# Performance work log

Measured on AMD Instinct MI355X. Metric: run time of the kernel, lower is better.

Reference implementation:

```python
import jax, jax.numpy as jnp
import numpy as np

GAIN = 1.0
EPS = 1e-08


def setup_inputs() -> dict:
    key = jax.random.key(0)
    k1, k2, k3 = jax.random.split(key, 3)
    B, H, W, Cin, Cout, K = 8, 64, 64, 512, 512, 3
    x = jax.random.normal(k1, (B, H, W, Cin), dtype=jnp.float32)
    style = jax.random.normal(k2, (B, Cin), dtype=jnp.float32)
    kernel = jax.random.normal(k3, (K, K, Cin, Cout), dtype=jnp.float32)
    return {"x": x, "style": style, "kernel": kernel}


def reference(x, style, kernel):
    # x: [B,H,W,Cin], style: [B,Cin], kernel: [K,K,Cin,Cout]
    B, H, W, Cin = x.shape
    K = kernel.shape[0]
    Cout = kernel.shape[-1]
    scale = GAIN / np.sqrt(K * K * Cin)

    # modulate: per-sample weights [B,K,K,Cin,Cout]
    ww = (scale * kernel)[None] * style[:, None, None, :, None]
    # demodulate
    sigma = jax.lax.rsqrt(jnp.sum(jnp.square(ww), axis=(1, 2, 3)) + EPS)  # [B,Cout]
    ww = ww * sigma[:, None, None, None, :]

    # grouped conv via batch->channel reshape (groups = B)
    x_nchw = jnp.transpose(x, (0, 3, 1, 2)).reshape(1, B * Cin, H, W)
    # weights to HWIO with per-sample groups stacked on output channels
    w = jnp.transpose(ww, (1, 2, 3, 0, 4)).reshape(K, K, Cin, B * Cout)
    out = jax.lax.conv_general_dilated(
        x_nchw, w,
        window_strides=(1, 1),
        padding='SAME',
        dimension_numbers=('NCHW', 'HWIO', 'NCHW'),
        feature_group_count=B,
    )  # [1, B*Cout, H, W]
    out = out.reshape(B, Cout, H, W)
    return jnp.transpose(out, (0, 2, 3, 1))  # [B,H,W,Cout]
```

## Files before the change

### kernel.cpp

```cpp
#include <hip/hip_runtime.h>

typedef __bf16 bf16x8 __attribute__((ext_vector_type(8)));
typedef float f32x4 __attribute__((ext_vector_type(4)));

#define SCALE_F 0.014731391274719738f
#define SCALE2_F 2.170138888888889e-4f

__device__ __forceinline__ ushort f2bf(float f) {
    uint x = __float_as_uint(f);
    uint r = (x + 0x7fffu + ((x >> 16) & 1u)) >> 16;
    return (ushort)r;
}

__device__ __forceinline__ void async_cp16(const void* g, void* l) {
    __builtin_amdgcn_global_load_lds(
        (const __attribute__((address_space(1))) void*)g,
        (__attribute__((address_space(3))) void*)l, 16, 0, 0);
}


__global__ void k_q(const float* __restrict__ kern, float* __restrict__ Q) {
    int idx = blockIdx.x * 256 + threadIdx.x;
    float s = 0.f;
#pragma unroll
    for (int t = 0; t < 9; ++t) { float v = kern[t * 262144 + idx]; s += v * v; }
    Q[idx] = s * SCALE2_F;
}

__global__ void k_sigma(const float* __restrict__ style, const float* __restrict__ Q,
                        float* __restrict__ sig) {
    __shared__ float s2[512];
    int b = blockIdx.x, t = threadIdx.x;
    float s = style[b * 512 + t];
    s2[t] = s * s;
    __syncthreads();
    float acc = 0.f;
#pragma unroll 8
    for (int ci = 0; ci < 512; ++ci) acc += s2[ci] * Q[ci * 512 + t];
    sig[b * 512 + t] = rsqrtf(acc + 1e-8f);
}

__global__ void k_wt(const float* __restrict__ kern, const float* __restrict__ style,
                     const float* __restrict__ sig, ushort* __restrict__ wT) {
    __shared__ ushort tile[64 * 65];
    int b = blockIdx.z, tap = blockIdx.y;
    int ci0 = (blockIdx.x >> 3) << 6, co0 = (blockIdx.x & 7) << 6;
    int t = threadIdx.x;
    int col = t & 63, rq = t >> 6;
#pragma unroll
    for (int r = 0; r < 16; ++r) {
        int ci_l = r * 4 + rq;
        float v = kern[(size_t)(tap * 512 + ci0 + ci_l) * 512 + co0 + col];
        float val = SCALE_F * v * style[b * 512 + ci0 + ci_l] * sig[b * 512 + co0 + col];
        tile[ci_l * 65 + col] = f2bf(val);
    }
    __syncthreads();
#pragma unroll
    for (int r = 0; r < 4; ++r) {
        int q = r * 256 + t;
        int co_l = q >> 4, ciq = (q & 15) << 2;
        uint lo = (uint)tile[ciq * 65 + co_l] | ((uint)tile[(ciq + 1) * 65 + co_l] << 16);
        uint hi = (uint)tile[(ciq + 2) * 65 + co_l] | ((uint)tile[(ciq + 3) * 65 + co_l] << 16);
        *(uint2*)(&wT[((size_t)(b * 9 + tap) * 512 + co0 + co_l) * 512 + ci0 + ciq]) =
            make_uint2(lo, hi);
    }
}

__global__ void k_xpad(const float* __restrict__ x, ushort* __restrict__ xp) {
    int idx = blockIdx.x * 256 + threadIdx.x;
    int pos = idx >> 6, e = idx & 63;
    int b = pos / 4356, rem = pos - b * 4356;
    int hp = rem / 66, wp = rem - hp * 66;
    int ci0 = e << 3;
    uint4 o = make_uint4(0u, 0u, 0u, 0u);
    if (hp >= 1 && hp <= 64 && wp >= 1 && wp <= 64) {
        const float4* s =
            (const float4*)(x + (((size_t)(b * 4096 + (hp - 1) * 64 + (wp - 1))) << 9) + ci0);
        float4 v0 = s[0], v1 = s[1];
        o.x = (uint)f2bf(v0.x) | ((uint)f2bf(v0.y) << 16);
        o.y = (uint)f2bf(v0.z) | ((uint)f2bf(v0.w) << 16);
        o.z = (uint)f2bf(v1.x) | ((uint)f2bf(v1.y) << 16);
        o.w = (uint)f2bf(v1.z) | ((uint)f2bf(v1.w) << 16);
    }
    *(uint4*)(xp + (((size_t)pos) << 9) + ci0) = o;
}

__global__ __launch_bounds__(512, 2) void conv_mfma(const ushort* __restrict__ xpad,
                                                    const ushort* __restrict__ wT,
                                                    float* __restrict__ out) {
    extern __shared__ char lds[];

    const int wg = blockIdx.x;
    const int swz = (wg & 7) * 32 + (wg >> 3);
    const int mt = swz & 15;
    const int nt = (swz >> 4) & 1;
    const int b = swz >> 5;

    const int tid = threadIdx.x;
    const int l = tid & 63, wv = tid >> 6;
    const int wm = (wv >> 2) * 128;
    const int wn = (wv & 3) * 64;
    const int ha = wv >> 2;
    const int hb = (wv & 3) >> 1;

    const int rl = l >> 3;
    const int g = (l & 7) ^ rl;
    const ushort* baseA[2][2];
    const ushort* baseB[2][2];
#pragma unroll
    for (int h = 0; h < 2; ++h)
#pragma unroll
        for (int i = 0; i < 2; ++i) {
            int rloc = wv * 16 + i * 8 + rl;
            int R = h * 128 + rloc;
            baseA[h][i] = xpad + ((size_t)((b * 66 + mt * 4 + (R >> 6)) * 66 + (R & 63))) * 512 + g * 8;
            baseB[h][i] = wT + ((size_t)(b * 9 * 512 + nt * 256 + R)) * 512 + g * 8;
        }
    const int so0 = (wv * 16) * 128;
    const int so1 = (wv * 16 + 8) * 128;

    auto offA = [](int t) -> int {
        int tap = t >> 3;
        int ky = (tap * 11) >> 5;
        int kx = tap - ky * 3;
        return (ky * 66 + kx) * 512 + ((t & 7) << 6);
    };
    auto offB = [](int t) -> int { return (t >> 3) * 262144 + ((t & 7) << 6); };

    auto stA = [&](int t, int h) {
        int ts = t > 71 ? 71 : t;
        int o = offA(ts);
        char* d = lds + (t & 1) * 32768 + h * 16384;
        async_cp16(baseA[h][0] + o, d + so0);
        async_cp16(baseA[h][1] + o, d + so1);
    };
    auto stB = [&](int t, int h) {
        int ts = t > 71 ? 71 : t;
        int o = offB(ts);
        char* d = lds + 65536 + (t & 1) * 32768 + h * 16384;
        async_cp16(baseB[h][0] + o, d + so0);
        async_cp16(baseB[h][1] + o, d + so1);
    };

    const int frow = l & 15;
    const int fchunk_base = l >> 4;
    const int fxor = l & 7;

    f32x4 acc[8][4];
#pragma unroll
    for (int mi = 0; mi < 8; ++mi)
#pragma unroll
        for (int ni = 0; ni < 4; ++ni) acc[mi][ni] = (f32x4){0.f, 0.f, 0.f, 0.f};

    bf16x8 bq[4][2];
    bf16x8 aqE[2][2], aqO[2][2];

    auto rdB = [&](const char* bB) {
#pragma unroll
        for (int kk = 0; kk < 2; ++kk)
#pragma unroll
            for (int ni = 0; ni < 4; ++ni) {
                int r = (wn & 64) + ni * 16 + frow;
                bq[ni][kk] = *(const bf16x8*)(bB + r * 128 +
                                              (((kk * 4 + fchunk_base) ^ fxor) * 16));
            }
    };
    auto rdA = [&](bf16x8 (&aq)[2][2], const char* aB, int q) {
#pragma unroll
        for (int m2 = 0; m2 < 2; ++m2)
#pragma unroll
            for (int kk = 0; kk < 2; ++kk) {
                int r = (2 * q + m2) * 16 + frow;
                aq[m2][kk] = *(const bf16x8*)(aB + r * 128 +
                                              (((kk * 4 + fchunk_base) ^ fxor) * 16));
            }
    };

#define FENCE_L4                                                        \
    {                                                                   \
        __builtin_amdgcn_sched_barrier(0);                              \
        asm volatile("s_waitcnt lgkmcnt(4)" ::: "memory");              \
        __builtin_amdgcn_s_barrier();                                   \
        __builtin_amdgcn_sched_barrier(0);                              \
    }
#define FENCE_L12                                                       \
    {                                                                   \
        __builtin_amdgcn_sched_barrier(0);                              \
        asm volatile("s_waitcnt lgkmcnt(12)" ::: "memory");             \
        __builtin_amdgcn_s_barrier();                                   \
        __builtin_amdgcn_sched_barrier(0);                              \
    }
#define FENCE_V4L4                                                      \
    {                                                                   \
        __builtin_amdgcn_sched_barrier(0);                              \
        asm volatile("s_waitcnt vmcnt(4) lgkmcnt(4)" ::: "memory");     \
        __builtin_amdgcn_s_barrier();                                   \
        __builtin_amdgcn_sched_barrier(0);                              \
    }
#define FENCE_V2L4                                                      \
    {                                                                   \
        __builtin_amdgcn_sched_barrier(0);                              \
        asm volatile("s_waitcnt vmcnt(2) lgkmcnt(4)" ::: "memory");     \
        __builtin_amdgcn_s_barrier();                                   \
        __builtin_amdgcn_sched_barrier(0);                              \
    }

#define MFMA16(Q, AQ)                                                                  \
    do {                                                                               \
        __builtin_amdgcn_s_setprio(1);                                                 \
        _Pragma("unroll") for (int kk = 0; kk < 2; ++kk)                               \
            _Pragma("unroll") for (int ni = 0; ni < 4; ++ni)                           \
                _Pragma("unroll") for (int m2 = 0; m2 < 2; ++m2)                       \
                    acc[2 * (Q) + m2][ni] = __builtin_amdgcn_mfma_f32_16x16x32_bf16(   \
                        (AQ)[m2][kk], bq[ni][kk], acc[2 * (Q) + m2][ni], 0, 0, 0);     \
        __builtin_amdgcn_s_setprio(0);                                                 \
    } while (0)

    const char* Ab0 = lds + ha * 16384;
    const char* Ab1 = lds + 32768 + ha * 16384;
    const char* Bb0 = lds + 65536 + hb * 16384;
    const char* Bb1 = lds + 98304 + hb * 16384;

    stA(0, 0); stA(0, 1);
    stB(0, 0); stB(0, 1);
    asm volatile("s_waitcnt vmcnt(0)" ::: "memory");
    __builtin_amdgcn_sched_barrier(0);
    __builtin_amdgcn_s_barrier();
    __builtin_amdgcn_sched_barrier(0);
    stB(1, 0); stB(1, 1);
    rdA(aqE, Ab0, 0);
    rdB(Bb0);

#pragma unroll 1
    for (int i = 0; i < 36; ++i) {
        const int T = 2 * i;
        rdA(aqO, Ab0, 1); stA(T + 1, 0);
        FENCE_L12; MFMA16(0, aqE);
        rdA(aqE, Ab0, 2); stA(T + 1, 1);
        FENCE_V4L4; MFMA16(1, aqO);
        rdA(aqO, Ab0, 3); stB(T + 2, 0);
        FENCE_V2L4; MFMA16(2, aqE);
        rdA(aqE, Ab1, 0); stB(T + 2, 1);
        FENCE_L4; MFMA16(3, aqO);
        rdB(Bb1);
        rdA(aqO, Ab1, 1); stA(T + 2, 0);
        FENCE_L12; MFMA16(0, aqE);
        rdA(aqE, Ab1, 2); stA(T + 2, 1);
        FENCE_L4; MFMA16(1, aqO);
        rdA(aqO, Ab1, 3); stB(T + 3, 0);
        FENCE_V2L4; MFMA16(2, aqE);
        rdA(aqE, Ab0, 0); stB(T + 3, 1);
        FENCE_L4; MFMA16(3, aqO);
        rdB(Bb0);
    }

    asm volatile("s_waitcnt vmcnt(0) lgkmcnt(0)" ::: "memory");

#pragma unroll
    for (int mi = 0; mi < 8; ++mi) {
#pragma unroll
        for (int ni = 0; ni < 4; ++ni) {
#pragma unroll
            for (int r = 0; r < 4; ++r) {
                int m = mt * 256 + wm + mi * 16 + (l >> 4) * 4 + r;
                int co = nt * 256 + wn + ni * 16 + (l & 15);
                out[(((size_t)(b * 4096 + m)) << 9) + co] = acc[mi][ni][r];
            }
        }
    }
#undef MFMA16
#undef FENCE_L4
#undef FENCE_L12
#undef FENCE_V4L4
#undef FENCE_V2L4
}


extern "C" void kernel_launch(void* const* d_in, const int* in_sizes, int n_in,
                              void* d_out, int out_size, void* d_ws, size_t ws_size,
                              hipStream_t stream) {
    const float* x = (const float*)d_in[0];
    const float* style = (const float*)d_in[1];
    const float* kern = (const float*)d_in[2];
    float* out = (float*)d_out;

    char* ws = (char*)d_ws;
    ushort* xpad = (ushort*)ws;
    ushort* wT = (ushort*)(ws + 35684352);
    float* Q = (float*)(ws + 35684352 + 37748736);
    float* sig = (float*)(ws + 35684352 + 37748736 + 1048576);

    (void)hipFuncSetAttribute((const void*)conv_mfma,
                              hipFuncAttributeMaxDynamicSharedMemorySize, 131072);

    k_q<<<1024, 256, 0, stream>>>(kern, Q);
    k_sigma<<<8, 512, 0, stream>>>(style, Q, sig);
    k_wt<<<dim3(64, 9, 8), 256, 0, stream>>>(kern, style, sig, wT);
    k_xpad<<<8712, 256, 0, stream>>>(x, xpad);
    conv_mfma<<<256, 512, 131072, stream>>>(xpad, wT, out);
}
```

Before: 180.1 us.

## Switch conv to 32x32x16 MFMA and load kernel tile once per batch

The main conv kernel replaces 16x16x32 bf16 MFMA tiles with 32x32x16 tiles. The LDS fragment reads, accumulators and output indexing are reorganised to match, which means fewer MFMA issues and fewer LDS reads per unit of work. Separately, the weight-modulation kernel now loads each fp32 kernel tile once and loops over the 8 batch samples, instead of launching one block per sample that re-reads the kernel. This cuts global reads but serialises the per-batch work inside fewer blocks, and the new fragment layout risks LDS bank conflicts.

```diff
diff --git a/kernel.cpp b/kernel.cpp
--- a/kernel.cpp
+++ b/kernel.cpp
@@ -1,7 +1,7 @@
 #include <hip/hip_runtime.h>
 
 typedef __bf16 bf16x8 __attribute__((ext_vector_type(8)));
-typedef float f32x4 __attribute__((ext_vector_type(4)));
+typedef float f32x16 __attribute__((ext_vector_type(16)));
 
 #define SCALE_F 0.014731391274719738f
 #define SCALE2_F 2.170138888888889e-4f
@@ -42,27 +42,33 @@
 
 __global__ void k_wt(const float* __restrict__ kern, const float* __restrict__ style,
                      const float* __restrict__ sig, ushort* __restrict__ wT) {
-    __shared__ ushort tile[64 * 65];
-    int b = blockIdx.z, tap = blockIdx.y;
+    __shared__ float tile[64][65];
+    int tap = blockIdx.y;
     int ci0 = (blockIdx.x >> 3) << 6, co0 = (blockIdx.x & 7) << 6;
     int t = threadIdx.x;
     int col = t & 63, rq = t >> 6;
 #pragma unroll
     for (int r = 0; r < 16; ++r) {
         int ci_l = r * 4 + rq;
-        float v = kern[(size_t)(tap * 512 + ci0 + ci_l) * 512 + co0 + col];
-        float val = SCALE_F * v * style[b * 512 + ci0 + ci_l] * sig[b * 512 + co0 + col];
-        tile[ci_l * 65 + col] = f2bf(val);
+        tile[ci_l][col] = SCALE_F * kern[(size_t)(tap * 512 + ci0 + ci_l) * 512 + co0 + col];
     }
     __syncthreads();
-#pragma unroll
-    for (int r = 0; r < 4; ++r) {
-        int q = r * 256 + t;
-        int co_l = q >> 4, ciq = (q & 15) << 2;
-        uint lo = (uint)tile[ciq * 65 + co_l] | ((uint)tile[(ciq + 1) * 65 + co_l] << 16);
-        uint hi = (uint)tile[(ciq + 2) * 65 + co_l] | ((uint)tile[(ciq + 3) * 65 + co_l] << 16);
-        *(uint2*)(&wT[((size_t)(b * 9 + tap) * 512 + co0 + co_l) * 512 + ci0 + ciq]) =
-            make_uint2(lo, hi);
+#pragma unroll 1
+    for (int b = 0; b < 8; ++b) {
+#pragma unroll
+        for (int r = 0; r < 4; ++r) {
+            int q = r * 256 + t;
+            int co_l = q >> 4, ciq = (q & 15) << 2;
+            float sg = sig[b * 512 + co0 + co_l];
+            float v0 = tile[ciq + 0][co_l] * style[b * 512 + ci0 + ciq + 0] * sg;
+            float v1 = tile[ciq + 1][co_l] * style[b * 512 + ci0 + ciq + 1] * sg;
+            float v2 = tile[ciq + 2][co_l] * style[b * 512 + ci0 + ciq + 2] * sg;
+            float v3 = tile[ciq + 3][co_l] * style[b * 512 + ci0 + ciq + 3] * sg;
+            uint lo = (uint)f2bf(v0) | ((uint)f2bf(v1) << 16);
+            uint hi = (uint)f2bf(v2) | ((uint)f2bf(v3) << 16);
+            *(uint2*)(&wT[((size_t)(b * 9 + tap) * 512 + co0 + co_l) * 512 + ci0 + ciq]) =
+                make_uint2(lo, hi);
+        }
     }
 }
 
@@ -99,7 +105,7 @@
     const int tid = threadIdx.x;
     const int l = tid & 63, wv = tid >> 6;
     const int wm = (wv >> 2) * 128;
-    const int wn = (wv & 3) * 64;
+    const int wnq = (wv & 3) * 64;
     const int ha = wv >> 2;
     const int hb = (wv & 3) >> 1;
 
@@ -142,38 +148,37 @@
         async_cp16(baseB[h][1] + o, d + so1);
     };
 
-    const int frow = l & 15;
-    const int fchunk_base = l >> 4;
-    const int fxor = l & 7;
-
-    f32x4 acc[8][4];
-#pragma unroll
-    for (int mi = 0; mi < 8; ++mi)
-#pragma unroll
-        for (int ni = 0; ni < 4; ++ni) acc[mi][ni] = (f32x4){0.f, 0.f, 0.f, 0.f};
-
-    bf16x8 bq[4][2];
-    bf16x8 aqE[2][2], aqO[2][2];
+    const int lrow = l & 31;
+    const int kgrp = l >> 5;
+
+    f32x16 acc[4][2];
+#pragma unroll
+    for (int mi = 0; mi < 4; ++mi)
+#pragma unroll
+        for (int ni = 0; ni < 2; ++ni)
+#pragma unroll
+            for (int r = 0; r < 16; ++r) acc[mi][ni][r] = 0.f;
+
+    bf16x8 bq[2][4];
+    bf16x8 aqE[4], aqO[4];
 
     auto rdB = [&](const char* bB) {
 #pragma unroll
-        for (int kk = 0; kk < 2; ++kk)
-#pragma unroll
-            for (int ni = 0; ni < 4; ++ni) {
-                int r = (wn & 64) + ni * 16 + frow;
-                bq[ni][kk] = *(const bf16x8*)(bB + r * 128 +
-                                              (((kk * 4 + fchunk_base) ^ fxor) * 16));
+        for (int s = 0; s < 4; ++s)
+#pragma unroll
+            for (int ni = 0; ni < 2; ++ni) {
+                int c = (wnq & 64) + ni * 32 + lrow;
+                bq[ni][s] = *(const bf16x8*)(bB + c * 128 +
+                                             (((s * 2 + kgrp) ^ (c & 7)) * 16));
             }
     };
-    auto rdA = [&](bf16x8 (&aq)[2][2], const char* aB, int q) {
-#pragma unroll
-        for (int m2 = 0; m2 < 2; ++m2)
-#pragma unroll
-            for (int kk = 0; kk < 2; ++kk) {
-                int r = (2 * q + m2) * 16 + frow;
-                aq[m2][kk] = *(const bf16x8*)(aB + r * 128 +
-                                              (((kk * 4 + fchunk_base) ^ fxor) * 16));
-            }
+    auto rdA = [&](bf16x8 (&aq)[4], const char* aB, int s) {
+#pragma unroll
+        for (int mi = 0; mi < 4; ++mi) {
+            int r = mi * 32 + lrow;
+            aq[mi] = *(const bf16x8*)(aB + r * 128 +
+                                      (((s * 2 + kgrp) ^ (r & 7)) * 16));
+        }
     };
 
 #define FENCE_L4                                                        \
@@ -205,14 +210,13 @@
         __builtin_amdgcn_sched_barrier(0);                              \
     }
 
-#define MFMA16(Q, AQ)                                                                  \
+#define MFMA8(S, AQ)                                                                   \
     do {                                                                               \
         __builtin_amdgcn_s_setprio(1);                                                 \
-        _Pragma("unroll") for (int kk = 0; kk < 2; ++kk)                               \
-            _Pragma("unroll") for (int ni = 0; ni < 4; ++ni)                           \
-                _Pragma("unroll") for (int m2 = 0; m2 < 2; ++m2)                       \
-                    acc[2 * (Q) + m2][ni] = __builtin_amdgcn_mfma_f32_16x16x32_bf16(   \
-                        (AQ)[m2][kk], bq[ni][kk], acc[2 * (Q) + m2][ni], 0, 0, 0);     \
+        _Pragma("unroll") for (int ni = 0; ni < 2; ++ni)                               \
+            _Pragma("unroll") for (int mi = 0; mi < 4; ++mi)                           \
+                acc[mi][ni] = __builtin_amdgcn_mfma_f32_32x32x16_bf16(                 \
+                    (AQ)[mi], bq[ni][S], acc[mi][ni], 0, 0, 0);                        \
         __builtin_amdgcn_s_setprio(0);                                                 \
     } while (0)
 
@@ -235,40 +239,40 @@
     for (int i = 0; i < 36; ++i) {
         const int T = 2 * i;
         rdA(aqO, Ab0, 1); stA(T + 1, 0);
-        FENCE_L12; MFMA16(0, aqE);
+        FENCE_L12; MFMA8(0, aqE);
         rdA(aqE, Ab0, 2); stA(T + 1, 1);
-        FENCE_V4L4; MFMA16(1, aqO);
+        FENCE_V4L4; MFMA8(1, aqO);
         rdA(aqO, Ab0, 3); stB(T + 2, 0);
-        FENCE_V2L4; MFMA16(2, aqE);
+        FENCE_V2L4; MFMA8(2, aqE);
         rdA(aqE, Ab1, 0); stB(T + 2, 1);
-        FENCE_L4; MFMA16(3, aqO);
+        FENCE_L4; MFMA8(3, aqO);
         rdB(Bb1);
         rdA(aqO, Ab1, 1); stA(T + 2, 0);
-        FENCE_L12; MFMA16(0, aqE);
+        FENCE_L12; MFMA8(0, aqE);
         rdA(aqE, Ab1, 2); stA(T + 2, 1);
-        FENCE_L4; MFMA16(1, aqO);
+        FENCE_L4; MFMA8(1, aqO);
         rdA(aqO, Ab1, 3); stB(T + 3, 0);
-        FENCE_V2L4; MFMA16(2, aqE);
+        FENCE_V2L4; MFMA8(2, aqE);
         rdA(aqE, Ab0, 0); stB(T + 3, 1);
-        FENCE_L4; MFMA16(3, aqO);
+        FENCE_L4; MFMA8(3, aqO);
         rdB(Bb0);
     }
 
     asm volatile("s_waitcnt vmcnt(0) lgkmcnt(0)" ::: "memory");
 
 #pragma unroll
-    for (int mi = 0; mi < 8; ++mi) {
-#pragma unroll
-        for (int ni = 0; ni < 4; ++ni) {
-#pragma unroll
-            for (int r = 0; r < 4; ++r) {
-                int m = mt * 256 + wm + mi * 16 + (l >> 4) * 4 + r;
-                int co = nt * 256 + wn + ni * 16 + (l & 15);
+    for (int mi = 0; mi < 4; ++mi) {
+#pragma unroll
+        for (int ni = 0; ni < 2; ++ni) {
+#pragma unroll
+            for (int r = 0; r < 16; ++r) {
+                int m = mt * 256 + wm + mi * 32 + (r & 3) + 8 * (r >> 2) + 4 * kgrp;
+                int co = nt * 256 + wnq + ni * 32 + lrow;
                 out[(((size_t)(b * 4096 + m)) << 9) + co] = acc[mi][ni][r];
             }
         }
     }
-#undef MFMA16
+#undef MFMA8
 #undef FENCE_L4
 #undef FENCE_L12
 #undef FENCE_V4L4
@@ -295,7 +299,7 @@
 
     k_q<<<1024, 256, 0, stream>>>(kern, Q);
     k_sigma<<<8, 512, 0, stream>>>(style, Q, sig);
-    k_wt<<<dim3(64, 9, 8), 256, 0, stream>>>(kern, style, sig, wT);
+    k_wt<<<dim3(64, 9), 256, 0, stream>>>(kern, style, sig, wT);
     k_xpad<<<8712, 256, 0, stream>>>(x, xpad);
     conv_mfma<<<256, 512, 131072, stream>>>(xpad, wT, out);
 }
```

New measurement: 198.5 us. +10.2%, slower.
